# Kernel tuning notes

Hardware: AMD Instinct MI355X
Metric: run time of the kernel (lower is better)

## Reference

```python
import math
import jax, jax.numpy as jnp
import numpy as np

B, T, C, HS = 8, 2048, 1024, 64

def setup_inputs() -> dict:
    key = jax.random.key(0)
    kx, kq, kk, kv = jax.random.split(key, 4)
    x = jax.random.normal(kx, (B, T, C), dtype=jnp.float32)
    # match nn.Linear init scale roughly: U(-1/sqrt(C), 1/sqrt(C))
    lim = 1.0 / math.sqrt(C)
    Wq = jax.random.uniform(kq, (C, HS), minval=-lim, maxval=lim, dtype=jnp.float32)
    Wk = jax.random.uniform(kk, (C, HS), minval=-lim, maxval=lim, dtype=jnp.float32)
    Wv = jax.random.uniform(kv, (C, HS), minval=-lim, maxval=lim, dtype=jnp.float32)
    return {"x": x, "Wq": Wq, "Wk": Wk, "Wv": Wv}

def reference(x, Wq, Wk, Wv):
    # NOTE: original scales by 1/sqrt(hs) where hs = x.shape[-1] = embd_size,
    # not head_size. Faithfully reproduced.
    Tlen = x.shape[1]
    scale = 1.0 / math.sqrt(x.shape[-1])
    q = jnp.einsum('btc,ch->bth', x, Wq)
    k = jnp.einsum('btc,ch->bth', x, Wk)
    v = jnp.einsum('btc,ch->bth', x, Wv)
    wei = jnp.einsum('bth,bsh->bts', q, k) * scale  # [B,T,T]
    causal = jnp.tril(jnp.ones((Tlen, Tlen), dtype=bool))
    wei = jnp.where(causal, wei, -jnp.inf)
    wei = jax.nn.softmax(wei, axis=-1)
    # dropout p=0.0 -> identity
    out = jnp.einsum('bts,bsh->bth', wei, v)  # [B,T,HS]
    return out
```

## Files before the change

kernel.cpp:

```cpp
#include <hip/hip_runtime.h>
#include <hip/hip_bf16.h>


#define T_SEQ 2048
#define C_DIM 1024
#define HS 64
#define BT 16384

typedef short s8v __attribute__((ext_vector_type(8)));
typedef float f4v __attribute__((ext_vector_type(4)));

__device__ inline unsigned short f2bf(float f) {
  union { float f; unsigned u; } a; a.f = f;
  unsigned r = a.u + 0x7fffu + ((a.u >> 16) & 1u);
  return (unsigned short)(r >> 16);
}

__device__ inline s8v cvt8(float4 v0, float4 v1) {
  union { __hip_bfloat162 h; unsigned u; } c0, c1, c2, c3;
  c0.h = __float22bfloat162_rn(make_float2(v0.x, v0.y));
  c1.h = __float22bfloat162_rn(make_float2(v0.z, v0.w));
  c2.h = __float22bfloat162_rn(make_float2(v1.x, v1.y));
  c3.h = __float22bfloat162_rn(make_float2(v1.z, v1.w));
  union { unsigned u[4]; s8v v; } r;
  r.u[0] = c0.u; r.u[1] = c1.u; r.u[2] = c2.u; r.u[3] = c3.u;
  return r.v;
}

__device__ inline void gl_lds16(const void* g, unsigned char* lds_base,
                                unsigned uniform_byte_off) {
  __builtin_amdgcn_global_load_lds(
      (const __attribute__((address_space(1))) unsigned int*)g,
      (__attribute__((address_space(3))) unsigned int*)(lds_base + uniform_byte_off),
      16, 0, 0);
}

__global__ __launch_bounds__(256) void wt_kernel(
    const float* __restrict__ Wq, const float* __restrict__ Wk,
    const float* __restrict__ Wv, unsigned short* __restrict__ wt) {
  __shared__ float tile[64][65];
  const int bid = blockIdx.x;
  const int mat = bid >> 4, kt = bid & 15;
  const float* W = (mat == 0) ? Wq : ((mat == 1) ? Wk : Wv);
  const int t = threadIdx.x;
  const int n = t & 63, kr = t >> 6;
#pragma unroll
  for (int j = 0; j < 16; ++j) {
    const int kl = j * 4 + kr;
    tile[kl][n] = W[(kt * 64 + kl) * HS + n];
  }
  __syncthreads();
  const int n2 = t >> 2, kp = t & 3;
  unsigned int* orow =
      (unsigned int*)(wt + (size_t)(mat * 64 + n2) * C_DIM + kt * 64);
#pragma unroll
  for (int i = 0; i < 8; ++i) {
    const int k0 = kp * 16 + i * 2;
    unsigned int lo = f2bf(tile[k0][n2]);
    unsigned int hi = f2bf(tile[k0 + 1][n2]);
    orow[kp * 8 + i] = lo | (hi << 16);
  }
}

__global__ __launch_bounds__(256) void qkv_kernel(
    const float* __restrict__ x, const unsigned short* __restrict__ wt,
    unsigned short* __restrict__ qws, unsigned short* __restrict__ kws,
    unsigned short* __restrict__ vtws) {
  __shared__ unsigned char abuf[2][8192];
  __shared__ unsigned char bbuf[2][24576];

  const int tid  = threadIdx.x;
  const int wv   = tid >> 6;
  const int lane = tid & 63;
  const int m    = lane & 15;
  const int quad = lane >> 4;
  const int row0 = blockIdx.x * 32;
  const int mh   = wv >> 1;
  const int ng   = (wv & 1) * 6;

  f4v acc[6];
#pragma unroll
  for (int j = 0; j < 6; ++j) acc[j] = (f4v)0.0f;

  const unsigned au = (unsigned)__builtin_amdgcn_readfirstlane(tid & 192) << 4;

  const float* agp[2];
#pragma unroll
  for (int j = 0; j < 2; ++j) {
    const int s = tid + j * 256;
    const int r = s >> 4, p = (s & 15) ^ (r & 15);
    agp[j] = x + (size_t)(row0 + r) * C_DIM + p * 4;
  }
  const unsigned short* bgp[6];
#pragma unroll
  for (int j = 0; j < 6; ++j) {
    const int s = tid + j * 256;
    const int n = s >> 3, p = (s & 7) ^ (n & 7);
    bgp[j] = wt + (size_t)n * C_DIM + p * 8;
  }

  int aoff[2][2];
#pragma unroll
  for (int c = 0; c < 2; ++c)
#pragma unroll
    for (int t = 0; t < 2; ++t)
      aoff[c][t] = (((mh * 16 + m) * 16) + ((c * 8 + 2 * quad + t) ^ m)) << 4;
  int boff[6][2];
#pragma unroll
  for (int j = 0; j < 6; ++j) {
    const int n = (ng + j) * 16 + m;
#pragma unroll
    for (int c = 0; c < 2; ++c)
      boff[j][c] = (n * 8 + ((c * 4 + quad) ^ (n & 7))) << 4;
  }

#define STAGE(buf, kk)                                                       \
  do {                                                                       \
    _Pragma("unroll") for (int j = 0; j < 2; ++j)                            \
        gl_lds16(agp[j] + (kk), abuf[buf], au + (unsigned)(j * 4096));       \
    _Pragma("unroll") for (int j = 0; j < 6; ++j)                            \
        gl_lds16(bgp[j] + (kk), bbuf[buf], au + (unsigned)(j * 4096));       \
  } while (0)

  STAGE(0, 0);
  for (int it = 0; it < 16; ++it) {
    __syncthreads();
    if (it < 15) STAGE((it + 1) & 1, (it + 1) * 64);
    const unsigned char* aB = abuf[it & 1];
    const unsigned char* bB = bbuf[it & 1];
#pragma unroll
    for (int c = 0; c < 2; ++c) {
      float4 xa = *(const float4*)(aB + aoff[c][0]);
      float4 xb = *(const float4*)(aB + aoff[c][1]);
      s8v a = cvt8(xa, xb);
#pragma unroll
      for (int j = 0; j < 6; ++j) {
        s8v b = *(const s8v*)(bB + boff[j][c]);
        acc[j] = __builtin_amdgcn_mfma_f32_16x16x32_bf16(a, b, acc[j], 0, 0, 0);
      }
    }
  }
#undef STAGE

  const float qscale = 1.4426950408889634f / 32.0f;
#pragma unroll
  for (int j = 0; j < 6; ++j) {
    const int nt = ng + j;
    const int mat = nt >> 2, ct = nt & 3;
    const int col = ct * 16 + m;
#pragma unroll
    for (int r = 0; r < 4; ++r) {
      const int row = row0 + mh * 16 + quad * 4 + r;
      const float v = acc[j][r];
      if (mat == 0) {
        qws[row * HS + col] = f2bf(v * qscale);
      } else if (mat == 1) {
        kws[row * HS + col] = f2bf(v);
      } else {
        const int bb = row >> 11, t = row & 2047;
        vtws[(bb * HS + col) * T_SEQ + t] = f2bf(v);
      }
    }
  }
}

union AttnSh {
  unsigned short p[8][16 * 72];
  float mo[8][16][64];
};

__global__ __launch_bounds__(512) void attn_kernel(
    const unsigned short* __restrict__ qws, const unsigned short* __restrict__ kws,
    const unsigned short* __restrict__ vtws, float* __restrict__ out) {
  __shared__ AttnSh sh;
  __shared__ float ml[8][16];

  const int tid  = threadIdx.x;
  const int wv   = tid >> 6;
  const int lane = tid & 63;
  const int m    = lane & 15;
  const int quad = lane >> 4;
  const int b    = blockIdx.x & 7;
  const int qt   = (T_SEQ / 16 - 1) - (blockIdx.x >> 3);
  const int r0   = qt * 16;
  const int gr0  = b * T_SEQ + r0;

  s8v aq0 = *(const s8v*)&qws[(size_t)(gr0 + m) * HS + quad * 8];
  s8v aq1 = *(const s8v*)&qws[(size_t)(gr0 + m) * HS + 32 + quad * 8];

  float li[4] = {0.f, 0.f, 0.f, 0.f};
  f4v o[4];
#pragma unroll
  for (int i = 0; i < 4; ++i) o[i] = (f4v)0.0f;

  const int nst = (r0 + 16 + 63) >> 6;
  unsigned short* pl = sh.p[wv];
  const int qrow_base = r0 + quad * 4;
  const unsigned short* kbase = kws + (size_t)b * T_SEQ * HS;
  const unsigned short* vbase = vtws + (size_t)b * HS * T_SEQ;

  for (int st = wv; st < nst; st += 8) {
    const int s0 = st * 64;

    s8v kf[4][2];
#pragma unroll
    for (int ns = 0; ns < 4; ++ns) {
      const unsigned short* kp = &kbase[(size_t)(s0 + ns * 16 + m) * HS + quad * 8];
      kf[ns][0] = *(const s8v*)kp;
      kf[ns][1] = *(const s8v*)(kp + 32);
    }
    s8v vf[4][2];
#pragma unroll
    for (int hn = 0; hn < 4; ++hn) {
      const unsigned short* vp = &vbase[(size_t)(hn * 16 + m) * T_SEQ + s0 + quad * 8];
      vf[hn][0] = *(const s8v*)vp;
      vf[hn][1] = *(const s8v*)(vp + 32);
    }

    f4v sacc[4];
#pragma unroll
    for (int ns = 0; ns < 4; ++ns) {
      f4v t = (f4v)0.0f;
      t = __builtin_amdgcn_mfma_f32_16x16x32_bf16(aq0, kf[ns][0], t, 0, 0, 0);
      t = __builtin_amdgcn_mfma_f32_16x16x32_bf16(aq1, kf[ns][1], t, 0, 0, 0);
      sacc[ns] = t;
    }

#pragma unroll
    for (int ns = 0; ns < 4; ++ns) {
      const int scol = s0 + ns * 16 + m;
#pragma unroll
      for (int r = 0; r < 4; ++r) {
        const float p = (scol > qrow_base + r) ? 0.f
                        : __builtin_amdgcn_exp2f(sacc[ns][r]);
        li[r] += p;
        pl[(quad * 4 + r) * 72 + ns * 16 + m] = f2bf(p);
      }
    }

    s8v ap0 = *(const s8v*)&pl[m * 72 + quad * 8];
    s8v ap1 = *(const s8v*)&pl[m * 72 + 32 + quad * 8];
#pragma unroll
    for (int hn = 0; hn < 4; ++hn) {
      o[hn] = __builtin_amdgcn_mfma_f32_16x16x32_bf16(ap0, vf[hn][0], o[hn], 0, 0, 0);
      o[hn] = __builtin_amdgcn_mfma_f32_16x16x32_bf16(ap1, vf[hn][1], o[hn], 0, 0, 0);
    }
  }

#pragma unroll
  for (int r = 0; r < 4; ++r) {
    float s = li[r];
    s += __shfl_xor(s, 1); s += __shfl_xor(s, 2);
    s += __shfl_xor(s, 4); s += __shfl_xor(s, 8);
    li[r] = s;
  }

  __syncthreads();

#pragma unroll
  for (int hn = 0; hn < 4; ++hn)
#pragma unroll
    for (int r = 0; r < 4; ++r)
      sh.mo[wv][quad * 4 + r][hn * 16 + m] = o[hn][r];
  if (m == 0) {
#pragma unroll
    for (int r = 0; r < 4; ++r) ml[wv][quad * 4 + r] = li[r];
  }
  __syncthreads();

  const int row = tid >> 5, cg = tid & 31;
  float ls = 0.f;
#pragma unroll
  for (int w = 0; w < 8; ++w) ls += ml[w][row];
  const float inv = 1.0f / ls;
  float rx = 0.f, ry = 0.f;
#pragma unroll
  for (int w = 0; w < 8; ++w) {
    float2 v = *(const float2*)&sh.mo[w][row][cg * 2];
    rx += v.x; ry += v.y;
  }
  float2 res; res.x = rx * inv; res.y = ry * inv;
  *(float2*)&out[(size_t)(gr0 + row) * HS + cg * 2] = res;
}

extern "C" void kernel_launch(void* const* d_in, const int* in_sizes, int n_in,
                              void* d_out, int out_size, void* d_ws, size_t ws_size,
                              hipStream_t stream) {
  const float* x  = (const float*)d_in[0];
  const float* Wq = (const float*)d_in[1];
  const float* Wk = (const float*)d_in[2];
  const float* Wv = (const float*)d_in[3];
  float* out = (float*)d_out;

  unsigned short* qws  = (unsigned short*)d_ws;
  unsigned short* kws  = qws + (size_t)BT * HS;
  unsigned short* vtws = kws + (size_t)BT * HS;
  unsigned short* wt   = vtws + (size_t)BT * HS;

  wt_kernel<<<dim3(48), dim3(256), 0, stream>>>(Wq, Wk, Wv, wt);
  qkv_kernel<<<dim3(BT / 32), dim3(256), 0, stream>>>(x, wt, qws, kws, vtws);
  attn_kernel<<<dim3(1024), dim3(512), 0, stream>>>(qws, kws, vtws, out);
}
```

Before: 151.1 us.

## Process 32 query rows per attention block and pack P stores via permuted V layout

Each attention workgroup now covers two 16-row query sub-tiles that share the same K and V fragments per 64-key step, so global K/V traffic is halved and the grid shrinks from 1024 to 512 blocks. The V^T workspace is written with a permuted key order inside each 64-key group. That lets each lane store its four P values as one packed 8-byte LDS write while still matching the MFMA operand order. The final reduction uses float4 accesses. The cost is more registers and LDS per block, fewer blocks to hide latency, and slightly more wasted masked work on the diagonal tile.

```diff
diff --git a/kernel.cpp b/kernel.cpp
--- a/kernel.cpp
+++ b/kernel.cpp
@@ -16,14 +16,16 @@
   return (unsigned short)(r >> 16);
 }
 
+__device__ inline unsigned pk2(float a, float b) {
+  union { __hip_bfloat162 h; unsigned u; } c;
+  c.h = __float22bfloat162_rn(make_float2(a, b));
+  return c.u;
+}
+
 __device__ inline s8v cvt8(float4 v0, float4 v1) {
-  union { __hip_bfloat162 h; unsigned u; } c0, c1, c2, c3;
-  c0.h = __float22bfloat162_rn(make_float2(v0.x, v0.y));
-  c1.h = __float22bfloat162_rn(make_float2(v0.z, v0.w));
-  c2.h = __float22bfloat162_rn(make_float2(v1.x, v1.y));
-  c3.h = __float22bfloat162_rn(make_float2(v1.z, v1.w));
   union { unsigned u[4]; s8v v; } r;
-  r.u[0] = c0.u; r.u[1] = c1.u; r.u[2] = c2.u; r.u[3] = c3.u;
+  r.u[0] = pk2(v0.x, v0.y); r.u[1] = pk2(v0.z, v0.w);
+  r.u[2] = pk2(v1.x, v1.y); r.u[3] = pk2(v1.z, v1.w);
   return r.v;
 }
 
@@ -158,22 +160,23 @@
         kws[row * HS + col] = f2bf(v);
       } else {
         const int bb = row >> 11, t = row & 2047;
-        vtws[(bb * HS + col) * T_SEQ + t] = f2bf(v);
+        const int tp = (t & ~63) | (((t & 15) << 2) | ((t >> 4) & 3));
+        vtws[(bb * HS + col) * T_SEQ + tp] = f2bf(v);
       }
     }
   }
 }
 
-union AttnSh {
-  unsigned short p[8][16 * 72];
-  float mo[8][16][64];
+union __align__(16) AttnSh {
+  unsigned short p[8][2][16 * 72];
+  float mo[8][32][64];
 };
 
 __global__ __launch_bounds__(512) void attn_kernel(
     const unsigned short* __restrict__ qws, const unsigned short* __restrict__ kws,
     const unsigned short* __restrict__ vtws, float* __restrict__ out) {
   __shared__ AttnSh sh;
-  __shared__ float ml[8][16];
+  __shared__ float ml[8][32];
 
   const int tid  = threadIdx.x;
   const int wv   = tid >> 6;
@@ -181,21 +184,27 @@
   const int m    = lane & 15;
   const int quad = lane >> 4;
   const int b    = blockIdx.x & 7;
-  const int qt   = (T_SEQ / 16 - 1) - (blockIdx.x >> 3);
-  const int r0   = qt * 16;
+  const int qi   = (T_SEQ / 32 - 1) - (blockIdx.x >> 3);
+  const int r0   = qi * 32;
   const int gr0  = b * T_SEQ + r0;
 
-  s8v aq0 = *(const s8v*)&qws[(size_t)(gr0 + m) * HS + quad * 8];
-  s8v aq1 = *(const s8v*)&qws[(size_t)(gr0 + m) * HS + 32 + quad * 8];
-
-  float li[4] = {0.f, 0.f, 0.f, 0.f};
-  f4v o[4];
-#pragma unroll
-  for (int i = 0; i < 4; ++i) o[i] = (f4v)0.0f;
-
-  const int nst = (r0 + 16 + 63) >> 6;
-  unsigned short* pl = sh.p[wv];
-  const int qrow_base = r0 + quad * 4;
+  const unsigned short* qp = qws + (size_t)(gr0 + m) * HS + quad * 8;
+  s8v aqA0 = *(const s8v*)qp;
+  s8v aqA1 = *(const s8v*)(qp + 32);
+  s8v aqB0 = *(const s8v*)(qp + 16 * HS);
+  s8v aqB1 = *(const s8v*)(qp + 16 * HS + 32);
+
+  float liA[4] = {0.f, 0.f, 0.f, 0.f};
+  float liB[4] = {0.f, 0.f, 0.f, 0.f};
+  f4v oA[4], oB[4];
+#pragma unroll
+  for (int i = 0; i < 4; ++i) { oA[i] = (f4v)0.0f; oB[i] = (f4v)0.0f; }
+
+  const int nst = (r0 + 32 + 63) >> 6;
+  unsigned short* plA = sh.p[wv][0];
+  unsigned short* plB = sh.p[wv][1];
+  const int qbA = r0 + quad * 4;
+  const int qbB = qbA + 16;
   const unsigned short* kbase = kws + (size_t)b * T_SEQ * HS;
   const unsigned short* vbase = vtws + (size_t)b * HS * T_SEQ;
 
@@ -217,42 +226,66 @@
       vf[hn][1] = *(const s8v*)(vp + 32);
     }
 
-    f4v sacc[4];
+    f4v sa[4], sb[4];
 #pragma unroll
     for (int ns = 0; ns < 4; ++ns) {
       f4v t = (f4v)0.0f;
-      t = __builtin_amdgcn_mfma_f32_16x16x32_bf16(aq0, kf[ns][0], t, 0, 0, 0);
-      t = __builtin_amdgcn_mfma_f32_16x16x32_bf16(aq1, kf[ns][1], t, 0, 0, 0);
-      sacc[ns] = t;
-    }
-
-#pragma unroll
-    for (int ns = 0; ns < 4; ++ns) {
-      const int scol = s0 + ns * 16 + m;
-#pragma unroll
-      for (int r = 0; r < 4; ++r) {
-        const float p = (scol > qrow_base + r) ? 0.f
-                        : __builtin_amdgcn_exp2f(sacc[ns][r]);
-        li[r] += p;
-        pl[(quad * 4 + r) * 72 + ns * 16 + m] = f2bf(p);
-      }
-    }
-
-    s8v ap0 = *(const s8v*)&pl[m * 72 + quad * 8];
-    s8v ap1 = *(const s8v*)&pl[m * 72 + 32 + quad * 8];
+      t = __builtin_amdgcn_mfma_f32_16x16x32_bf16(aqA0, kf[ns][0], t, 0, 0, 0);
+      t = __builtin_amdgcn_mfma_f32_16x16x32_bf16(aqA1, kf[ns][1], t, 0, 0, 0);
+      sa[ns] = t;
+      f4v u = (f4v)0.0f;
+      u = __builtin_amdgcn_mfma_f32_16x16x32_bf16(aqB0, kf[ns][0], u, 0, 0, 0);
+      u = __builtin_amdgcn_mfma_f32_16x16x32_bf16(aqB1, kf[ns][1], u, 0, 0, 0);
+      sb[ns] = u;
+    }
+
+    const int sm = s0 + m;
+#pragma unroll
+    for (int r = 0; r < 4; ++r) {
+      const int qr = qbA + r;
+      const float p0 = (sm      > qr) ? 0.f : __builtin_amdgcn_exp2f(sa[0][r]);
+      const float p1 = (sm + 16 > qr) ? 0.f : __builtin_amdgcn_exp2f(sa[1][r]);
+      const float p2 = (sm + 32 > qr) ? 0.f : __builtin_amdgcn_exp2f(sa[2][r]);
+      const float p3 = (sm + 48 > qr) ? 0.f : __builtin_amdgcn_exp2f(sa[3][r]);
+      liA[r] += (p0 + p1) + (p2 + p3);
+      *(uint2*)&plA[(quad * 4 + r) * 72 + m * 4] =
+          make_uint2(pk2(p0, p1), pk2(p2, p3));
+    }
+#pragma unroll
+    for (int r = 0; r < 4; ++r) {
+      const int qr = qbB + r;
+      const float p0 = (sm      > qr) ? 0.f : __builtin_amdgcn_exp2f(sb[0][r]);
+      const float p1 = (sm + 16 > qr) ? 0.f : __builtin_amdgcn_exp2f(sb[1][r]);
+      const float p2 = (sm + 32 > qr) ? 0.f : __builtin_amdgcn_exp2f(sb[2][r]);
+      const float p3 = (sm + 48 > qr) ? 0.f : __builtin_amdgcn_exp2f(sb[3][r]);
+      liB[r] += (p0 + p1) + (p2 + p3);
+      *(uint2*)&plB[(quad * 4 + r) * 72 + m * 4] =
+          make_uint2(pk2(p0, p1), pk2(p2, p3));
+    }
+
+    s8v apA0 = *(const s8v*)&plA[m * 72 + quad * 8];
+    s8v apA1 = *(const s8v*)&plA[m * 72 + 32 + quad * 8];
+    s8v apB0 = *(const s8v*)&plB[m * 72 + quad * 8];
+    s8v apB1 = *(const s8v*)&plB[m * 72 + 32 + quad * 8];
 #pragma unroll
     for (int hn = 0; hn < 4; ++hn) {
-      o[hn] = __builtin_amdgcn_mfma_f32_16x16x32_bf16(ap0, vf[hn][0], o[hn], 0, 0, 0);
-      o[hn] = __builtin_amdgcn_mfma_f32_16x16x32_bf16(ap1, vf[hn][1], o[hn], 0, 0, 0);
+      oA[hn] = __builtin_amdgcn_mfma_f32_16x16x32_bf16(apA0, vf[hn][0], oA[hn], 0, 0, 0);
+      oA[hn] = __builtin_amdgcn_mfma_f32_16x16x32_bf16(apA1, vf[hn][1], oA[hn], 0, 0, 0);
+      oB[hn] = __builtin_amdgcn_mfma_f32_16x16x32_bf16(apB0, vf[hn][0], oB[hn], 0, 0, 0);
+      oB[hn] = __builtin_amdgcn_mfma_f32_16x16x32_bf16(apB1, vf[hn][1], oB[hn], 0, 0, 0);
     }
   }
 
 #pragma unroll
   for (int r = 0; r < 4; ++r) {
-    float s = li[r];
+    float s = liA[r];
     s += __shfl_xor(s, 1); s += __shfl_xor(s, 2);
     s += __shfl_xor(s, 4); s += __shfl_xor(s, 8);
-    li[r] = s;
+    liA[r] = s;
+    float u = liB[r];
+    u += __shfl_xor(u, 1); u += __shfl_xor(u, 2);
+    u += __shfl_xor(u, 4); u += __shfl_xor(u, 8);
+    liB[r] = u;
   }
 
   __syncthreads();
@@ -260,27 +293,33 @@
 #pragma unroll
   for (int hn = 0; hn < 4; ++hn)
 #pragma unroll
-    for (int r = 0; r < 4; ++r)
-      sh.mo[wv][quad * 4 + r][hn * 16 + m] = o[hn][r];
+    for (int r = 0; r < 4; ++r) {
+      sh.mo[wv][quad * 4 + r][hn * 16 + m] = oA[hn][r];
+      sh.mo[wv][16 + quad * 4 + r][hn * 16 + m] = oB[hn][r];
+    }
   if (m == 0) {
 #pragma unroll
-    for (int r = 0; r < 4; ++r) ml[wv][quad * 4 + r] = li[r];
+    for (int r = 0; r < 4; ++r) {
+      ml[wv][quad * 4 + r] = liA[r];
+      ml[wv][16 + quad * 4 + r] = liB[r];
+    }
   }
   __syncthreads();
 
-  const int row = tid >> 5, cg = tid & 31;
+  const int row = tid >> 4, c4 = (tid & 15) * 4;
   float ls = 0.f;
 #pragma unroll
   for (int w = 0; w < 8; ++w) ls += ml[w][row];
   const float inv = 1.0f / ls;
-  float rx = 0.f, ry = 0.f;
+  float ax = 0.f, ay = 0.f, az = 0.f, aw = 0.f;
 #pragma unroll
   for (int w = 0; w < 8; ++w) {
-    float2 v = *(const float2*)&sh.mo[w][row][cg * 2];
-    rx += v.x; ry += v.y;
-  }
-  float2 res; res.x = rx * inv; res.y = ry * inv;
-  *(float2*)&out[(size_t)(gr0 + row) * HS + cg * 2] = res;
+    float4 v = *(const float4*)&sh.mo[w][row][c4];
+    ax += v.x; ay += v.y; az += v.z; aw += v.w;
+  }
+  float4 res;
+  res.x = ax * inv; res.y = ay * inv; res.z = az * inv; res.w = aw * inv;
+  *(float4*)&out[(size_t)(gr0 + row) * HS + c4] = res;
 }
 
 extern "C" void kernel_launch(void* const* d_in, const int* in_sizes, int n_in,
@@ -299,5 +338,5 @@
 
   wt_kernel<<<dim3(48), dim3(256), 0, stream>>>(Wq, Wk, Wv, wt);
   qkv_kernel<<<dim3(BT / 32), dim3(256), 0, stream>>>(x, wt, qws, kws, vtws);
-  attn_kernel<<<dim3(1024), dim3(512), 0, stream>>>(qws, kws, vtws, out);
-}
+  attn_kernel<<<dim3(512), dim3(512), 0, stream>>>(qws, kws, vtws, out);
+}
```

Result: faster. 137.7 us (-8.9%).
